# Kernel tuning notes

Hardware: AMD Instinct MI355X
Metric: run time of the kernel (lower is better)

## Reference

```python
import jax, jax.numpy as jnp
import numpy as np

INPUT_CHANNELS = 3

def setup_inputs() -> dict:
    key = jax.random.key(0)
    k1, k2 = jax.random.split(key)
    B, N, C = 16, 4096, 3
    x = jax.random.normal(k1, (B, N, C), dtype=jnp.float32)
    y = jax.random.normal(k2, (B, N, C), dtype=jnp.float32)
    return {"x": x, "y": y}

def reference(x, y):
    # Slice to input_channels (identity here since C == INPUT_CHANNELS)
    x = x[:, :, :INPUT_CHANNELS]
    y = y[:, :, :INPUT_CHANNELS]
    # pdist[b, i, j] = ||x_i||^2 + ||y_j||^2 - 2 x_i . y_j  -> squared euclidean
    x2 = jnp.sum(x * x, axis=-1)  # [B, N]
    y2 = jnp.sum(y * y, axis=-1)  # [B, N]
    zz = jnp.einsum('bic,bjc->bij', x, y)  # [B, N, N]
    pdist = x2[:, :, None] + y2[:, None, :] - 2.0 * zz
    # min over axis 1: nearest x for each y; min over axis 2: nearest y for each x
    loss = jnp.mean(jnp.min(pdist, axis=1)) + jnp.mean(jnp.min(pdist, axis=2))
    return loss
```

## Files before the change

kernel.cpp:

```cpp
#include <hip/hip_runtime.h>
#include <stdint.h>

#define BATCH 16
#define NPTS  4096
#define TOT   (BATCH * NPTS)
#define TWOTOT (2 * TOT)
#define JSEG  8

typedef float f4 __attribute__((ext_vector_type(4)));
typedef float f32x4 __attribute__((ext_vector_type(4)));
typedef short bh8 __attribute__((ext_vector_type(8)));
typedef uint32_t u32;
typedef unsigned short u16;

__device__ __forceinline__ u16 bfr(float f) {
    union { float f; u32 u; } v; v.f = f;
    u32 r = v.u + 0x7FFF + ((v.u >> 16) & 1);
    return (u16)(r >> 16);
}
__device__ __forceinline__ float bfback(u16 h) {
    union { u32 u; float f; } v; v.u = ((u32)h) << 16; return v.f;
}
#define BF16_ONE ((u16)0x3F80)

#define MIN3r(d, a, b, c) \
    asm("v_min3_f32 %0, %1, %2, %3" : "=v"(d) : "v"(a), "v"(b), "v"(c))
#define MIN3a(acc, u, v) \
    asm("v_min3_f32 %0, %1, %2, %0" : "+v"(acc) : "v"(u), "v"(v))

__global__ __launch_bounds__(256) void pack_mfma(const float* __restrict__ x,
                                                 const float* __restrict__ y,
                                                 u16* __restrict__ Arec,
                                                 u16* __restrict__ Brec,
                                                 float* __restrict__ out) {
    int idx = blockIdx.x * 256 + threadIdx.x;
    if (idx == 0) out[0] = 0.0f;

    bool isx = idx < TOT;
    int r = isx ? idx : (idx - TOT);
    const float* src = isx ? x : y;
    float a = src[r * 3 + 0];
    float b = src[r * 3 + 1];
    float c = src[r * 3 + 2];
    float s2 = fmaf(a, a, fmaf(b, b, c * c));
    u16 s2h = bfr(s2);
    u16 s2l = bfr(s2 - bfback(s2h));

    union { u16 h[16]; f4 v[2]; } rec;
    if (isx) {
        float ax = -2.0f * a, ay = -2.0f * b, az = -2.0f * c;
        u16 ahx = bfr(ax), ahy = bfr(ay), ahz = bfr(az);
        u16 alx = bfr(ax - bfback(ahx));
        u16 aly = bfr(ay - bfback(ahy));
        u16 alz = bfr(az - bfback(ahz));
        rec.h[0] = ahx;  rec.h[1] = ahy;  rec.h[2] = ahz;
        rec.h[3] = ahx;  rec.h[4] = ahy;  rec.h[5] = ahz;
        rec.h[6] = alx;  rec.h[7] = aly;
        rec.h[8] = alz;  rec.h[9] = s2h;  rec.h[10] = s2l;
        rec.h[11] = BF16_ONE; rec.h[12] = BF16_ONE;
        rec.h[13] = 0; rec.h[14] = 0; rec.h[15] = 0;
        f4* dst = (f4*)(Arec + (size_t)r * 16);
        dst[0] = rec.v[0]; dst[1] = rec.v[1];
    } else {
        u16 yhx = bfr(a), yhy = bfr(b), yhz = bfr(c);
        u16 ylx = bfr(a - bfback(yhx));
        u16 yly = bfr(b - bfback(yhy));
        u16 ylz = bfr(c - bfback(yhz));
        rec.h[0] = yhx;  rec.h[1] = yhy;  rec.h[2] = yhz;
        rec.h[3] = ylx;  rec.h[4] = yly;  rec.h[5] = ylz;
        rec.h[6] = yhx;  rec.h[7] = yhy;
        rec.h[8] = yhz;  rec.h[9] = BF16_ONE; rec.h[10] = BF16_ONE;
        rec.h[11] = s2h; rec.h[12] = s2l;
        rec.h[13] = 0; rec.h[14] = 0; rec.h[15] = 0;
        f4* dst = (f4*)(Brec + (size_t)r * 16);
        dst[0] = rec.v[0]; dst[1] = rec.v[1];
    }
}

#define DSRL(dst, base, imm) \
    asm volatile("ds_read_b128 %0, %1 offset:" imm : "=v"(dst) : "v"(base))

#define WAITL(cnt, slot) do { \
    asm volatile("s_waitcnt lgkmcnt(" cnt ")" : "+v"(slot)); \
    __builtin_amdgcn_sched_barrier(0); \
} while (0)

#define MF4(P, BB) do { \
    P##0 = __builtin_amdgcn_mfma_f32_16x16x32_bf16(af0, BB, zc, 0, 0, 0); \
    P##1 = __builtin_amdgcn_mfma_f32_16x16x32_bf16(af1, BB, zc, 0, 0, 0); \
    P##2 = __builtin_amdgcn_mfma_f32_16x16x32_bf16(af2, BB, zc, 0, 0, 0); \
    P##3 = __builtin_amdgcn_mfma_f32_16x16x32_bf16(af3, BB, zc, 0, 0, 0); \
} while (0)

#define COLV(cv, P) do { \
    float t0,t1,t2,t3,t4,t5,t6; \
    MIN3r(t0, P##0[0], P##0[1], P##0[2]); \
    MIN3r(t1, P##0[3], P##1[0], P##1[1]); \
    MIN3r(t2, P##1[2], P##1[3], P##2[0]); \
    MIN3r(t3, P##2[1], P##2[2], P##2[3]); \
    MIN3r(t4, P##3[0], P##3[1], P##3[2]); \
    t5 = fminf(P##3[3], t0); \
    MIN3r(t6, t1, t2, t3); \
    MIN3r(cv, t4, t5, t6); \
} while (0)

#define EPI2(PA, PB) do { \
    MIN3a(r00, PA##0[0], PB##0[0]); MIN3a(r01, PA##0[1], PB##0[1]); \
    MIN3a(r02, PA##0[2], PB##0[2]); MIN3a(r03, PA##0[3], PB##0[3]); \
    MIN3a(r10, PA##1[0], PB##1[0]); MIN3a(r11, PA##1[1], PB##1[1]); \
    MIN3a(r12, PA##1[2], PB##1[2]); MIN3a(r13, PA##1[3], PB##1[3]); \
    MIN3a(r20, PA##2[0], PB##2[0]); MIN3a(r21, PA##2[1], PB##2[1]); \
    MIN3a(r22, PA##2[2], PB##2[2]); MIN3a(r23, PA##2[3], PB##2[3]); \
    MIN3a(r30, PA##3[0], PB##3[0]); MIN3a(r31, PA##3[1], PB##3[1]); \
    MIN3a(r32, PA##3[2], PB##3[2]); MIN3a(r33, PA##3[3], PB##3[3]); \
    float cvA, cvB; \
    COLV(cvA, PA); COLV(cvB, PB); \
    asm volatile("ds_min_f32 %0, %1" :: "v"(cma), "v"(cvA)); \
    asm volatile("ds_min_f32 %0, %1 offset:64" :: "v"(cma), "v"(cvB)); \
    cma += 128; \
} while (0)

__global__ __launch_bounds__(256) void chamfer_mfma(const u16* __restrict__ Arec,
                                                    const u16* __restrict__ Brec,
                                                    float* __restrict__ colpart,
                                                    float* __restrict__ rowpart) {
    constexpr int QLEN = NPTS / JSEG;
    __shared__ u16  Bst[QLEN * 16];
    __shared__ float colmin[QLEN];

    int bid  = blockIdx.x;
    int b    = bid >> 7;
    int ic   = (bid >> 3) & 15;
    int jseg = bid & 7;
    int tid  = threadIdx.x;
    int wv   = tid >> 6, lane = tid & 63;
    int lg   = lane >> 4, lm = lane & 15;

    int i0 = ic * 256 + wv * 64;
    int j0 = jseg * QLEN;

    {
        const f4* src = (const f4*)(Brec + ((size_t)b * NPTS + j0) * 16);
        f4* dst = (f4*)Bst;
        int t4 = tid * 4;
        f4 v0 = src[t4 + 0], v1 = src[t4 + 1], v2 = src[t4 + 2], v3 = src[t4 + 3];
        dst[t4 + 0] = v0; dst[t4 + 1] = v1; dst[t4 + 2] = v2; dst[t4 + 3] = v3;
    }
    for (int i = tid; i < QLEN; i += 256) colmin[i] = 3.4e38f;

    bh8 af0, af1, af2, af3;
    {
        bh8 z8 = {0, 0, 0, 0, 0, 0, 0, 0};
        const u16* ab = Arec + ((size_t)b * NPTS + i0 + lm) * 16 + lg * 8;
        af0 = (lg < 2) ? *(const bh8*)(ab + 0)   : z8;
        af1 = (lg < 2) ? *(const bh8*)(ab + 256) : z8;
        af2 = (lg < 2) ? *(const bh8*)(ab + 512) : z8;
        af3 = (lg < 2) ? *(const bh8*)(ab + 768) : z8;
    }
    __syncthreads();

    u32 lofs = (u32)(uintptr_t)&Bst[0] + ((lg < 2) ? (u32)(lm * 32 + lg * 16) : 0u);
    u32 cma  = (u32)(uintptr_t)&colmin[0] + (u32)lm * 4;

    f32x4 zc = {0.f, 0.f, 0.f, 0.f};
    float r00=3.4e38f, r01=3.4e38f, r02=3.4e38f, r03=3.4e38f;
    float r10=3.4e38f, r11=3.4e38f, r12=3.4e38f, r13=3.4e38f;
    float r20=3.4e38f, r21=3.4e38f, r22=3.4e38f, r23=3.4e38f;
    float r30=3.4e38f, r31=3.4e38f, r32=3.4e38f, r33=3.4e38f;

    f32x4 aA0, aA1, aA2, aA3, aB0, aB1, aB2, aB3;
    bh8 s0, s1, s2, s3, s4, s5;

    DSRL(s0, lofs, "0");    DSRL(s1, lofs, "512");
    DSRL(s2, lofs, "1024"); DSRL(s3, lofs, "1536");
    DSRL(s4, lofs, "2048"); DSRL(s5, lofs, "2560");

    WAITL("5", s0); MF4(aA, s0); DSRL(s0, lofs, "3072");
    WAITL("5", s1); MF4(aB, s1); DSRL(s1, lofs, "3584");
    EPI2(aA, aB);

    u32 lofs2 = lofs + 4096;
    #pragma unroll 1
    for (int k = 0; k < 4; ++k) {
        WAITL("7", s2); MF4(aA, s2); DSRL(s2, lofs2, "0");
        WAITL("7", s3); MF4(aB, s3); DSRL(s3, lofs2, "512");
        EPI2(aA, aB);
        WAITL("7", s4); MF4(aA, s4); DSRL(s4, lofs2, "1024");
        WAITL("7", s5); MF4(aB, s5); DSRL(s5, lofs2, "1536");
        EPI2(aA, aB);
        WAITL("7", s0); MF4(aA, s0); DSRL(s0, lofs2, "2048");
        WAITL("7", s1); MF4(aB, s1); DSRL(s1, lofs2, "2560");
        EPI2(aA, aB);
        lofs2 += 3072;
    }
    WAITL("7", s2); MF4(aA, s2);
    WAITL("6", s3); MF4(aB, s3);
    EPI2(aA, aB);
    WAITL("7", s4); MF4(aA, s4);
    WAITL("5", s5); MF4(aB, s5);
    EPI2(aA, aB);
    WAITL("4", s0); MF4(aA, s0);
    WAITL("0", s1); MF4(aB, s1);
    EPI2(aA, aB);

    #define RRED(r) { r = fminf(r, __shfl_xor(r, 1)); r = fminf(r, __shfl_xor(r, 2)); \
                      r = fminf(r, __shfl_xor(r, 4)); r = fminf(r, __shfl_xor(r, 8)); }
    RRED(r00) RRED(r01) RRED(r02) RRED(r03)
    RRED(r10) RRED(r11) RRED(r12) RRED(r13)
    RRED(r20) RRED(r21) RRED(r22) RRED(r23)
    RRED(r30) RRED(r31) RRED(r32) RRED(r33)
    if (lm == 0) {
        float* rp = rowpart + (size_t)jseg * TOT + (size_t)b * NPTS + i0 + lg * 4;
        rp[0]  = r00; rp[1]  = r01; rp[2]  = r02; rp[3]  = r03;
        rp[16] = r10; rp[17] = r11; rp[18] = r12; rp[19] = r13;
        rp[32] = r20; rp[33] = r21; rp[34] = r22; rp[35] = r23;
        rp[48] = r30; rp[49] = r31; rp[50] = r32; rp[51] = r33;
    }

    __syncthreads();
    for (int j = tid; j < QLEN; j += 256)
        colpart[(size_t)ic * TOT + (size_t)b * NPTS + j0 + j] = colmin[j];
}

__global__ __launch_bounds__(256) void chamfer_pass2(const float* __restrict__ rowpart,
                                                     const float* __restrict__ colpart,
                                                     float* __restrict__ out) {
    int t = blockIdx.x * 256 + threadIdx.x;
    float mr = rowpart[t];
    #pragma unroll
    for (int s = 1; s < JSEG; ++s) mr = fminf(mr, rowpart[(size_t)s * TOT + t]);
    float mc = colpart[t];
    #pragma unroll
    for (int ic = 1; ic < 16; ++ic) mc = fminf(mc, colpart[(size_t)ic * TOT + t]);

    float s = mr + mc;
    #pragma unroll
    for (int off = 32; off; off >>= 1) s += __shfl_down(s, off);
    __shared__ float red[4];
    int lane = threadIdx.x & 63, wid = threadIdx.x >> 6;
    if (lane == 0) red[wid] = s;
    __syncthreads();
    if (threadIdx.x == 0) {
        float tot = (red[0] + red[1]) + (red[2] + red[3]);
        atomicAdd(out, tot * (1.0f / (float)TOT));
    }
}

__global__ __launch_bounds__(256) void chamfer_direct(const float* __restrict__ x,
                                                      const float* __restrict__ y,
                                                      float* __restrict__ out) {
    int blk = blockIdx.x;
    int dir = blk >> 8;
    int t = blk & 255;
    int b = t >> 4;
    int chunk = t & 15;
    const float* __restrict__ P = (dir ? y : x) + (b * NPTS + chunk * 256) * 3;
    const float* __restrict__ Q = (dir ? x : y) + b * NPTS * 3;
    float px = P[threadIdx.x * 3 + 0];
    float py = P[threadIdx.x * 3 + 1];
    float pz = P[threadIdx.x * 3 + 2];
    float b0 = 3.4e38f, b1 = 3.4e38f, b2 = 3.4e38f, b3 = 3.4e38f;
    for (int j = 0; j < NPTS; j += 4) {
        #pragma unroll
        for (int u = 0; u < 4; ++u) {
            float dx = px - Q[(j + u) * 3 + 0];
            float dy = py - Q[(j + u) * 3 + 1];
            float dz = pz - Q[(j + u) * 3 + 2];
            float d = fmaf(dx, dx, fmaf(dy, dy, dz * dz));
            if (u == 0) b0 = fminf(b0, d);
            if (u == 1) b1 = fminf(b1, d);
            if (u == 2) b2 = fminf(b2, d);
            if (u == 3) b3 = fminf(b3, d);
        }
    }
    float best = fminf(fminf(b0, b1), fminf(b2, b3));
    float v = best;
    #pragma unroll
    for (int off = 32; off; off >>= 1) v += __shfl_down(v, off);
    __shared__ float red[4];
    int lane = threadIdx.x & 63, wid = threadIdx.x >> 6;
    if (lane == 0) red[wid] = v;
    __syncthreads();
    if (threadIdx.x == 0) {
        float s = (red[0] + red[1]) + (red[2] + red[3]);
        atomicAdd(out, s * (1.0f / (float)TOT));
    }
}

__global__ void zero_kernel(float* out) { out[0] = 0.0f; }

extern "C" void kernel_launch(void* const* d_in, const int* in_sizes, int n_in,
                              void* d_out, int out_size, void* d_ws, size_t ws_size,
                              hipStream_t stream) {
    const float* x = (const float*)d_in[0];
    const float* y = (const float*)d_in[1];
    float* out = (float*)d_out;

    size_t need = (size_t)10 << 20;
    if (ws_size >= need) {
        u16*   Arec    = (u16*)d_ws;
        u16*   Brec    = (u16*)((char*)d_ws + ((size_t)2 << 20));
        float* colpart = (float*)((char*)d_ws + ((size_t)4 << 20));
        float* rowpart = (float*)((char*)d_ws + ((size_t)8 << 20));
        hipLaunchKernelGGL(pack_mfma, dim3(TWOTOT / 256), dim3(256), 0, stream,
                           x, y, Arec, Brec, out);
        hipLaunchKernelGGL(chamfer_mfma, dim3(16 * 16 * JSEG), dim3(256), 0, stream,
                           Arec, Brec, colpart, rowpart);
        hipLaunchKernelGGL(chamfer_pass2, dim3(TOT / 256), dim3(256), 0, stream,
                           rowpart, colpart, out);
    } else {
        hipLaunchKernelGGL(zero_kernel, dim3(1), dim3(1), 0, stream, out);
        hipLaunchKernelGGL(chamfer_direct, dim3(512), dim3(256), 0, stream, x, y, out);
    }
}
```

Measured before the change: 43.31 us.

## Double per-wave row tile to 128 points, halving blocks and column partials

Each wave now covers 128 x-points (8 MFMA A fragments) instead of 64, so each B fragment loaded from LDS feeds 8 MFMAs and the column min per B tile becomes one ds_min instead of two. Grid blocks drop from 2048 to 1024, the column-partial count drops from 16 to 8, and the pass-2 reduction and workspace shrink to match. The LDS prefetch pipeline is restructured to 4 in-flight slots. This trades fewer LDS reads and atomics for higher register pressure (8 accumulators plus 8 products) and half as many blocks, which may lower occupancy.

Result: no change. 42.87 us (-1.0%).

```diff
diff --git a/kernel.cpp b/kernel.cpp
--- a/kernel.cpp
+++ b/kernel.cpp
@@ -25,8 +25,6 @@
 
 #define MIN3r(d, a, b, c) \
     asm("v_min3_f32 %0, %1, %2, %3" : "=v"(d) : "v"(a), "v"(b), "v"(c))
-#define MIN3a(acc, u, v) \
-    asm("v_min3_f32 %0, %1, %2, %0" : "+v"(acc) : "v"(u), "v"(v))
 
 __global__ __launch_bounds__(256) void pack_mfma(const float* __restrict__ x,
                                                  const float* __restrict__ y,
@@ -85,39 +83,45 @@
     __builtin_amdgcn_sched_barrier(0); \
 } while (0)
 
-#define MF4(P, BB) do { \
-    P##0 = __builtin_amdgcn_mfma_f32_16x16x32_bf16(af0, BB, zc, 0, 0, 0); \
-    P##1 = __builtin_amdgcn_mfma_f32_16x16x32_bf16(af1, BB, zc, 0, 0, 0); \
-    P##2 = __builtin_amdgcn_mfma_f32_16x16x32_bf16(af2, BB, zc, 0, 0, 0); \
-    P##3 = __builtin_amdgcn_mfma_f32_16x16x32_bf16(af3, BB, zc, 0, 0, 0); \
+#define MF8(BB) do { \
+    p0 = __builtin_amdgcn_mfma_f32_16x16x32_bf16(af0, BB, zc, 0, 0, 0); \
+    p1 = __builtin_amdgcn_mfma_f32_16x16x32_bf16(af1, BB, zc, 0, 0, 0); \
+    p2 = __builtin_amdgcn_mfma_f32_16x16x32_bf16(af2, BB, zc, 0, 0, 0); \
+    p3 = __builtin_amdgcn_mfma_f32_16x16x32_bf16(af3, BB, zc, 0, 0, 0); \
+    p4 = __builtin_amdgcn_mfma_f32_16x16x32_bf16(af4, BB, zc, 0, 0, 0); \
+    p5 = __builtin_amdgcn_mfma_f32_16x16x32_bf16(af5, BB, zc, 0, 0, 0); \
+    p6 = __builtin_amdgcn_mfma_f32_16x16x32_bf16(af6, BB, zc, 0, 0, 0); \
+    p7 = __builtin_amdgcn_mfma_f32_16x16x32_bf16(af7, BB, zc, 0, 0, 0); \
 } while (0)
 
-#define COLV(cv, P) do { \
-    float t0,t1,t2,t3,t4,t5,t6; \
-    MIN3r(t0, P##0[0], P##0[1], P##0[2]); \
-    MIN3r(t1, P##0[3], P##1[0], P##1[1]); \
-    MIN3r(t2, P##1[2], P##1[3], P##2[0]); \
-    MIN3r(t3, P##2[1], P##2[2], P##2[3]); \
-    MIN3r(t4, P##3[0], P##3[1], P##3[2]); \
-    t5 = fminf(P##3[3], t0); \
-    MIN3r(t6, t1, t2, t3); \
-    MIN3r(cv, t4, t5, t6); \
-} while (0)
-
-#define EPI2(PA, PB) do { \
-    MIN3a(r00, PA##0[0], PB##0[0]); MIN3a(r01, PA##0[1], PB##0[1]); \
-    MIN3a(r02, PA##0[2], PB##0[2]); MIN3a(r03, PA##0[3], PB##0[3]); \
-    MIN3a(r10, PA##1[0], PB##1[0]); MIN3a(r11, PA##1[1], PB##1[1]); \
-    MIN3a(r12, PA##1[2], PB##1[2]); MIN3a(r13, PA##1[3], PB##1[3]); \
-    MIN3a(r20, PA##2[0], PB##2[0]); MIN3a(r21, PA##2[1], PB##2[1]); \
-    MIN3a(r22, PA##2[2], PB##2[2]); MIN3a(r23, PA##2[3], PB##2[3]); \
-    MIN3a(r30, PA##3[0], PB##3[0]); MIN3a(r31, PA##3[1], PB##3[1]); \
-    MIN3a(r32, PA##3[2], PB##3[2]); MIN3a(r33, PA##3[3], PB##3[3]); \
-    float cvA, cvB; \
-    COLV(cvA, PA); COLV(cvB, PB); \
-    asm volatile("ds_min_f32 %0, %1" :: "v"(cma), "v"(cvA)); \
-    asm volatile("ds_min_f32 %0, %1 offset:64" :: "v"(cma), "v"(cvB)); \
-    cma += 128; \
+#define EPI1() do { \
+    ra0[0]=fminf(ra0[0],p0[0]); ra0[1]=fminf(ra0[1],p0[1]); ra0[2]=fminf(ra0[2],p0[2]); ra0[3]=fminf(ra0[3],p0[3]); \
+    ra1[0]=fminf(ra1[0],p1[0]); ra1[1]=fminf(ra1[1],p1[1]); ra1[2]=fminf(ra1[2],p1[2]); ra1[3]=fminf(ra1[3],p1[3]); \
+    ra2[0]=fminf(ra2[0],p2[0]); ra2[1]=fminf(ra2[1],p2[1]); ra2[2]=fminf(ra2[2],p2[2]); ra2[3]=fminf(ra2[3],p2[3]); \
+    ra3[0]=fminf(ra3[0],p3[0]); ra3[1]=fminf(ra3[1],p3[1]); ra3[2]=fminf(ra3[2],p3[2]); ra3[3]=fminf(ra3[3],p3[3]); \
+    ra4[0]=fminf(ra4[0],p4[0]); ra4[1]=fminf(ra4[1],p4[1]); ra4[2]=fminf(ra4[2],p4[2]); ra4[3]=fminf(ra4[3],p4[3]); \
+    ra5[0]=fminf(ra5[0],p5[0]); ra5[1]=fminf(ra5[1],p5[1]); ra5[2]=fminf(ra5[2],p5[2]); ra5[3]=fminf(ra5[3],p5[3]); \
+    ra6[0]=fminf(ra6[0],p6[0]); ra6[1]=fminf(ra6[1],p6[1]); ra6[2]=fminf(ra6[2],p6[2]); ra6[3]=fminf(ra6[3],p6[3]); \
+    ra7[0]=fminf(ra7[0],p7[0]); ra7[1]=fminf(ra7[1],p7[1]); ra7[2]=fminf(ra7[2],p7[2]); ra7[3]=fminf(ra7[3],p7[3]); \
+    float t0,t1,t2,t3,t4,t5,t6,t7,t8,t9,t10,u0,u1,u2,u3,cv; \
+    MIN3r(t0, p0[0], p0[1], p0[2]); \
+    MIN3r(t1, p0[3], p1[0], p1[1]); \
+    MIN3r(t2, p1[2], p1[3], p2[0]); \
+    MIN3r(t3, p2[1], p2[2], p2[3]); \
+    MIN3r(t4, p3[0], p3[1], p3[2]); \
+    MIN3r(t5, p3[3], p4[0], p4[1]); \
+    MIN3r(t6, p4[2], p4[3], p5[0]); \
+    MIN3r(t7, p5[1], p5[2], p5[3]); \
+    MIN3r(t8, p6[0], p6[1], p6[2]); \
+    MIN3r(t9, p6[3], p7[0], p7[1]); \
+    MIN3r(t10, p7[2], p7[3], t0); \
+    MIN3r(u0, t1, t2, t3); \
+    MIN3r(u1, t4, t5, t6); \
+    MIN3r(u2, t7, t8, t9); \
+    MIN3r(u3, t10, u0, u1); \
+    cv = fminf(u2, u3); \
+    asm volatile("ds_min_f32 %0, %1" :: "v"(cma), "v"(cv)); \
+    cma += 64; \
 } while (0)
 
 __global__ __launch_bounds__(256) void chamfer_mfma(const u16* __restrict__ Arec,
@@ -129,14 +133,14 @@
     __shared__ float colmin[QLEN];
 
     int bid  = blockIdx.x;
-    int b    = bid >> 7;
-    int ic   = (bid >> 3) & 15;
+    int b    = bid >> 6;
+    int ic   = (bid >> 3) & 7;
     int jseg = bid & 7;
     int tid  = threadIdx.x;
     int wv   = tid >> 6, lane = tid & 63;
     int lg   = lane >> 4, lm = lane & 15;
 
-    int i0 = ic * 256 + wv * 64;
+    int i0 = ic * 512 + wv * 128;
     int j0 = jseg * QLEN;
 
     {
@@ -148,14 +152,18 @@
     }
     for (int i = tid; i < QLEN; i += 256) colmin[i] = 3.4e38f;
 
-    bh8 af0, af1, af2, af3;
+    bh8 af0, af1, af2, af3, af4, af5, af6, af7;
     {
         bh8 z8 = {0, 0, 0, 0, 0, 0, 0, 0};
         const u16* ab = Arec + ((size_t)b * NPTS + i0 + lm) * 16 + lg * 8;
-        af0 = (lg < 2) ? *(const bh8*)(ab + 0)   : z8;
-        af1 = (lg < 2) ? *(const bh8*)(ab + 256) : z8;
-        af2 = (lg < 2) ? *(const bh8*)(ab + 512) : z8;
-        af3 = (lg < 2) ? *(const bh8*)(ab + 768) : z8;
+        af0 = (lg < 2) ? *(const bh8*)(ab + 0)    : z8;
+        af1 = (lg < 2) ? *(const bh8*)(ab + 256)  : z8;
+        af2 = (lg < 2) ? *(const bh8*)(ab + 512)  : z8;
+        af3 = (lg < 2) ? *(const bh8*)(ab + 768)  : z8;
+        af4 = (lg < 2) ? *(const bh8*)(ab + 1024) : z8;
+        af5 = (lg < 2) ? *(const bh8*)(ab + 1280) : z8;
+        af6 = (lg < 2) ? *(const bh8*)(ab + 1536) : z8;
+        af7 = (lg < 2) ? *(const bh8*)(ab + 1792) : z8;
     }
     __syncthreads();
 
@@ -163,59 +171,45 @@
     u32 cma  = (u32)(uintptr_t)&colmin[0] + (u32)lm * 4;
 
     f32x4 zc = {0.f, 0.f, 0.f, 0.f};
-    float r00=3.4e38f, r01=3.4e38f, r02=3.4e38f, r03=3.4e38f;
-    float r10=3.4e38f, r11=3.4e38f, r12=3.4e38f, r13=3.4e38f;
-    float r20=3.4e38f, r21=3.4e38f, r22=3.4e38f, r23=3.4e38f;
-    float r30=3.4e38f, r31=3.4e38f, r32=3.4e38f, r33=3.4e38f;
-
-    f32x4 aA0, aA1, aA2, aA3, aB0, aB1, aB2, aB3;
-    bh8 s0, s1, s2, s3, s4, s5;
+    f32x4 big = {3.4e38f, 3.4e38f, 3.4e38f, 3.4e38f};
+    f32x4 ra0 = big, ra1 = big, ra2 = big, ra3 = big;
+    f32x4 ra4 = big, ra5 = big, ra6 = big, ra7 = big;
+    f32x4 p0, p1, p2, p3, p4, p5, p6, p7;
+    bh8 s0, s1, s2, s3;
 
     DSRL(s0, lofs, "0");    DSRL(s1, lofs, "512");
     DSRL(s2, lofs, "1024"); DSRL(s3, lofs, "1536");
-    DSRL(s4, lofs, "2048"); DSRL(s5, lofs, "2560");
-
-    WAITL("5", s0); MF4(aA, s0); DSRL(s0, lofs, "3072");
-    WAITL("5", s1); MF4(aB, s1); DSRL(s1, lofs, "3584");
-    EPI2(aA, aB);
+
+    WAITL("3", s0); MF8(s0); DSRL(s0, lofs, "2048"); EPI1();
+    WAITL("4", s1); MF8(s1); DSRL(s1, lofs, "2560"); EPI1();
+    WAITL("5", s2); MF8(s2); DSRL(s2, lofs, "3072"); EPI1();
+    WAITL("6", s3); MF8(s3); DSRL(s3, lofs, "3584"); EPI1();
 
     u32 lofs2 = lofs + 4096;
     #pragma unroll 1
-    for (int k = 0; k < 4; ++k) {
-        WAITL("7", s2); MF4(aA, s2); DSRL(s2, lofs2, "0");
-        WAITL("7", s3); MF4(aB, s3); DSRL(s3, lofs2, "512");
-        EPI2(aA, aB);
-        WAITL("7", s4); MF4(aA, s4); DSRL(s4, lofs2, "1024");
-        WAITL("7", s5); MF4(aB, s5); DSRL(s5, lofs2, "1536");
-        EPI2(aA, aB);
-        WAITL("7", s0); MF4(aA, s0); DSRL(s0, lofs2, "2048");
-        WAITL("7", s1); MF4(aB, s1); DSRL(s1, lofs2, "2560");
-        EPI2(aA, aB);
-        lofs2 += 3072;
-    }
-    WAITL("7", s2); MF4(aA, s2);
-    WAITL("6", s3); MF4(aB, s3);
-    EPI2(aA, aB);
-    WAITL("7", s4); MF4(aA, s4);
-    WAITL("5", s5); MF4(aB, s5);
-    EPI2(aA, aB);
-    WAITL("4", s0); MF4(aA, s0);
-    WAITL("0", s1); MF4(aB, s1);
-    EPI2(aA, aB);
+    for (int k = 0; k < 6; ++k) {
+        WAITL("7", s0); MF8(s0); DSRL(s0, lofs2, "0");    EPI1();
+        WAITL("7", s1); MF8(s1); DSRL(s1, lofs2, "512");  EPI1();
+        WAITL("7", s2); MF8(s2); DSRL(s2, lofs2, "1024"); EPI1();
+        WAITL("7", s3); MF8(s3); DSRL(s3, lofs2, "1536"); EPI1();
+        lofs2 += 2048;
+    }
+    WAITL("7", s0); MF8(s0); EPI1();
+    WAITL("6", s1); MF8(s1); EPI1();
+    WAITL("5", s2); MF8(s2); EPI1();
+    WAITL("4", s3); MF8(s3); EPI1();
 
     #define RRED(r) { r = fminf(r, __shfl_xor(r, 1)); r = fminf(r, __shfl_xor(r, 2)); \
                       r = fminf(r, __shfl_xor(r, 4)); r = fminf(r, __shfl_xor(r, 8)); }
-    RRED(r00) RRED(r01) RRED(r02) RRED(r03)
-    RRED(r10) RRED(r11) RRED(r12) RRED(r13)
-    RRED(r20) RRED(r21) RRED(r22) RRED(r23)
-    RRED(r30) RRED(r31) RRED(r32) RRED(r33)
-    if (lm == 0) {
-        float* rp = rowpart + (size_t)jseg * TOT + (size_t)b * NPTS + i0 + lg * 4;
-        rp[0]  = r00; rp[1]  = r01; rp[2]  = r02; rp[3]  = r03;
-        rp[16] = r10; rp[17] = r11; rp[18] = r12; rp[19] = r13;
-        rp[32] = r20; rp[33] = r21; rp[34] = r22; rp[35] = r23;
-        rp[48] = r30; rp[49] = r31; rp[50] = r32; rp[51] = r33;
-    }
+    float* rp = rowpart + (size_t)jseg * TOT + (size_t)b * NPTS + i0 + lg * 4;
+    #define RSTORE(pf, fi) do { \
+        float a = pf[0], bq = pf[1], c = pf[2], d = pf[3]; \
+        RRED(a) RRED(bq) RRED(c) RRED(d) \
+        if (lm == 0) { rp[fi*16 + 0] = a; rp[fi*16 + 1] = bq; \
+                       rp[fi*16 + 2] = c; rp[fi*16 + 3] = d; } \
+    } while (0)
+    RSTORE(ra0, 0); RSTORE(ra1, 1); RSTORE(ra2, 2); RSTORE(ra3, 3);
+    RSTORE(ra4, 4); RSTORE(ra5, 5); RSTORE(ra6, 6); RSTORE(ra7, 7);
 
     __syncthreads();
     for (int j = tid; j < QLEN; j += 256)
@@ -231,7 +225,7 @@
     for (int s = 1; s < JSEG; ++s) mr = fminf(mr, rowpart[(size_t)s * TOT + t]);
     float mc = colpart[t];
     #pragma unroll
-    for (int ic = 1; ic < 16; ++ic) mc = fminf(mc, colpart[(size_t)ic * TOT + t]);
+    for (int ic = 1; ic < 8; ++ic) mc = fminf(mc, colpart[(size_t)ic * TOT + t]);
 
     float s = mr + mc;
     #pragma unroll
@@ -296,15 +290,15 @@
     const float* y = (const float*)d_in[1];
     float* out = (float*)d_out;
 
-    size_t need = (size_t)10 << 20;
+    size_t need = (size_t)8 << 20;
     if (ws_size >= need) {
         u16*   Arec    = (u16*)d_ws;
         u16*   Brec    = (u16*)((char*)d_ws + ((size_t)2 << 20));
         float* colpart = (float*)((char*)d_ws + ((size_t)4 << 20));
-        float* rowpart = (float*)((char*)d_ws + ((size_t)8 << 20));
+        float* rowpart = (float*)((char*)d_ws + ((size_t)6 << 20));
         hipLaunchKernelGGL(pack_mfma, dim3(TWOTOT / 256), dim3(256), 0, stream,
                            x, y, Arec, Brec, out);
-        hipLaunchKernelGGL(chamfer_mfma, dim3(16 * 16 * JSEG), dim3(256), 0, stream,
+        hipLaunchKernelGGL(chamfer_mfma, dim3(16 * 8 * JSEG), dim3(256), 0, stream,
                            Arec, Brec, colpart, rowpart);
         hipLaunchKernelGGL(chamfer_pass2, dim3(TOT / 256), dim3(256), 0, stream,
                            rowpart, colpart, out);
```
